# Optimization experiments

Hardware: AMD Instinct MI355X
Metric: run time of the kernel (lower is better)

The kernel has to match this reference:

```python
import jax, jax.numpy as jnp
import numpy as np

DIM = 1024
NUM_HEADS = 16
HEAD_DIM = DIM // NUM_HEADS
SCALE = HEAD_DIM ** (-0.5)


def setup_inputs() -> dict:
    key = jax.random.key(0)
    k_x, k_qkv, k_ow, k_ob = jax.random.split(key, 4)
    x = jax.random.normal(k_x, (4, 2048, DIM), dtype=jnp.float32)
    # nn.Linear(dim, 3*dim, bias=False): store as [dim, 3*dim] for x @ W
    w_qkv = jax.random.normal(k_qkv, (DIM, 3 * DIM), dtype=jnp.float32) * (DIM ** -0.5)
    w_out = jax.random.normal(k_ow, (DIM, DIM), dtype=jnp.float32) * (DIM ** -0.5)
    b_out = jax.random.normal(k_ob, (DIM,), dtype=jnp.float32) * 0.02
    return {"x": x, "w_qkv": w_qkv, "w_out": w_out, "b_out": b_out}


def reference(x, w_qkv, w_out, b_out):
    B, S, D = x.shape
    H, Hd = NUM_HEADS, HEAD_DIM
    qkv = x @ w_qkv                                  # [B, S, 3*D]
    # rearrange 'b s (v h d) -> v b h s d'
    qkv = qkv.reshape(B, S, 3, H, Hd).transpose(2, 0, 3, 1, 4)
    q, k, v = qkv[0], qkv[1], qkv[2]                 # each [B, H, S, Hd]
    scores = jnp.einsum('bhqd,bhkd->bhqk', q, k) * SCALE
    attn = jax.nn.softmax(scores, axis=-1)
    out = jnp.einsum('bhqk,bhkd->bhqd', attn, v)     # [B, H, S, Hd]
    out = out.transpose(0, 2, 1, 3).reshape(B, S, D)  # 'b h s d -> b s (h d)'
    return out @ w_out + b_out
```

## Files before the change

### kernel.cpp

```cpp
#include <hip/hip_runtime.h>
#include <hip/hip_bf16.h>
#include <stdint.h>

typedef __bf16 bf16_t;
typedef __bf16 bf16x4 __attribute__((ext_vector_type(4)));
typedef __bf16 bf16x8 __attribute__((ext_vector_type(8)));
typedef float f32x4 __attribute__((ext_vector_type(4)));
typedef unsigned short u16;

#define L2E 1.4426950408889634f
#define MC 69.249473f

__device__ __forceinline__ void async_load16(const bf16_t* g, bf16_t* l) {
  __builtin_amdgcn_global_load_lds(
      (__attribute__((address_space(1))) uint32_t*)g,
      (__attribute__((address_space(3))) uint32_t*)l, 16, 0, 0);
}

__global__ void detect_k(const uint16_t* __restrict__ x, int* __restrict__ flag) {
  if (threadIdx.x == 0 && blockIdx.x == 0) {
    int bad = 0;
    for (int i = 0; i < 256; ++i) {
      uint16_t h = x[2 * i];
      int e = (h >> 7) & 0xFF;
      if (e == 0 || e >= 0xBD) bad++;
    }
    *flag = (bad > 32) ? 1 : 0;
  }
}

__global__ void convert_k(const void* __restrict__ in, bf16_t* __restrict__ out,
                          int n, const int* __restrict__ flag) {
  const int f = *flag;
  const int i0 = blockIdx.x * blockDim.x + threadIdx.x;
  const int stride = gridDim.x * blockDim.x;
  if (f) {
    const float* p = (const float*)in;
    for (int i = i0; i < n; i += stride) {
      float v = p[i];
      v = (v == v) ? v : 0.f;
      v = fminf(fmaxf(v, -1e6f), 1e6f);
      out[i] = (bf16_t)v;
    }
  } else {
    const bf16_t* p = (const bf16_t*)in;
    for (int i = i0; i < n; i += stride) {
      float v = (float)p[i];
      v = (v == v) ? v : 0.f;
      v = fminf(fmaxf(v, -1e6f), 1e6f);
      out[i] = (bf16_t)v;
    }
  }
}

__global__ __launch_bounds__(256) void wtrans_k(const void* __restrict__ in,
                                                bf16_t* __restrict__ out, int R,
                                                int C, const int* __restrict__ flag) {
  __shared__ u16 tile[64][65];
  const int f = *flag;
  const int tr = blockIdx.y * 64, tc = blockIdx.x * 64;
  const int t = threadIdx.x;
#pragma unroll
  for (int i = 0; i < 16; ++i) {
    int idx = i * 256 + t, r = idx >> 6, c = idx & 63;
    float v;
    if (f)
      v = ((const float*)in)[(size_t)(tr + r) * C + tc + c];
    else
      v = (float)((const bf16_t*)in)[(size_t)(tr + r) * C + tc + c];
    v = (v == v) ? v : 0.f;
    v = fminf(fmaxf(v, -1e6f), 1e6f);
    bf16_t b = (bf16_t)v;
    tile[r][c] = *(u16*)&b;
  }
  __syncthreads();
#pragma unroll
  for (int i = 0; i < 16; ++i) {
    int idx = i * 256 + t, r = idx >> 6, c = idx & 63;
    ((u16*)out)[(size_t)(tc + r) * R + tr + c] = tile[c][r];
  }
}

__device__ __forceinline__ void gemm_bt_mainloop(
    const bf16_t* __restrict__ A, const bf16_t* __restrict__ Bt, int K, int m0,
    int n0, bf16_t* As, bf16_t* Bs, f32x4 acc[4][4]) {
  const int t = threadIdx.x, lane = t & 63, w = t >> 6;
  const int l15 = lane & 15, quad = lane >> 4;
  const int wm = (w >> 1) * 64, wn = (w & 1) * 64;
  const int srow = w * 16 + (lane >> 2);
  const int sk = (lane & 3) * 8;
  const bf16_t* gA = A + (size_t)(m0 + srow) * K + sk;
  const bf16_t* gB = Bt + (size_t)(n0 + srow) * K + sk;
  bf16_t* lA = As + w * 512;
  bf16_t* lB = Bs + w * 512;
  const size_t gstep = (size_t)64 * K;

  for (int kt = 0; kt < K; kt += 32) {
    __syncthreads();
    async_load16(gA, lA);
    async_load16(gA + gstep, lA + 2048);
    async_load16(gB, lB);
    async_load16(gB + gstep, lB + 2048);
    gA += 32;
    gB += 32;
    __syncthreads();
    bf16x8 af[4], bfr[4];
#pragma unroll
    for (int f = 0; f < 4; ++f) {
      af[f] = *(const bf16x8*)(As + (wm + f * 16 + l15) * 32 + quad * 8);
      bfr[f] = *(const bf16x8*)(Bs + (wn + f * 16 + l15) * 32 + quad * 8);
    }
#pragma unroll
    for (int i = 0; i < 4; ++i)
#pragma unroll
      for (int j = 0; j < 4; ++j)
        acc[i][j] =
            __builtin_amdgcn_mfma_f32_16x16x32_bf16(af[i], bfr[j], acc[i][j], 0, 0, 0);
  }
}

__global__ __launch_bounds__(256) void qkv_gemm_k(const bf16_t* __restrict__ X,
                                                  const bf16_t* __restrict__ WqT,
                                                  bf16_t* __restrict__ qo,
                                                  bf16_t* __restrict__ ko,
                                                  bf16_t* __restrict__ vo) {
  __shared__ __align__(16) bf16_t As[128 * 32];
  __shared__ __align__(16) bf16_t Bs[128 * 32];
  const int m0 = blockIdx.y * 128, n0 = blockIdx.x * 128;
  f32x4 acc[4][4];
  const f32x4 z = {0.f, 0.f, 0.f, 0.f};
#pragma unroll
  for (int i = 0; i < 4; ++i)
#pragma unroll
    for (int j = 0; j < 4; ++j) acc[i][j] = z;
  gemm_bt_mainloop(X, WqT, 1024, m0, n0, As, Bs, acc);

  const int lane = threadIdx.x & 63, w = threadIdx.x >> 6;
  const int l15 = lane & 15, quad = lane >> 4;
  const int wm = (w >> 1) * 64, wn = (w & 1) * 64;
#pragma unroll
  for (int j = 0; j < 4; ++j) {
    const int gnb = n0 + wn + j * 16;
    const int vi = gnb >> 10;
    const int rem = gnb & 1023;
    const int h = rem >> 6;
    const int d = (rem & 63) + l15;
    const float scale = (vi == 0) ? 0.125f : 1.0f;
    bf16_t* dst = (vi == 0) ? qo : ((vi == 1) ? ko : vo);
#pragma unroll
    for (int i = 0; i < 4; ++i) {
#pragma unroll
      for (int r = 0; r < 4; ++r) {
        const int gm = m0 + wm + i * 16 + quad * 4 + r;
        const int b = gm >> 11, s = gm & 2047;
        dst[(((size_t)(b * 16 + h) * 2048 + s) << 6) + d] =
            (bf16_t)(acc[i][j][r] * scale);
      }
    }
  }
}

__global__ __launch_bounds__(256) void vtrans_k(const u16* __restrict__ in,
                                                u16* __restrict__ out) {
  __shared__ u16 tile[64][65];
  const int bh = blockIdx.y, st = blockIdx.x;
  const u16* src = in + ((size_t)bh * 2048 + st * 64) * 64;
  u16* dst = out + (size_t)bh * 64 * 2048 + st * 64;
  const int t = threadIdx.x;
#pragma unroll
  for (int i = 0; i < 16; ++i) {
    int idx = i * 256 + t, r = idx >> 6, c = idx & 63;
    tile[r][c] = src[(size_t)r * 64 + c];
  }
  __syncthreads();
#pragma unroll
  for (int i = 0; i < 16; ++i) {
    int idx = i * 256 + t, r = idx >> 6, c = idx & 63;
    dst[(size_t)r * 2048 + c] = tile[c][r];
  }
}

__global__ __launch_bounds__(256) void out_gemm_k(const bf16_t* __restrict__ Ain,
                                                  const bf16_t* __restrict__ WoT,
                                                  const bf16_t* __restrict__ bias,
                                                  void* __restrict__ outp,
                                                  const int* __restrict__ flag) {
  __shared__ __align__(16) bf16_t As[128 * 32];
  __shared__ __align__(16) bf16_t Bs[128 * 32];
  const int m0 = blockIdx.y * 128, n0 = blockIdx.x * 128;
  f32x4 acc[4][4];
  const f32x4 z = {0.f, 0.f, 0.f, 0.f};
#pragma unroll
  for (int i = 0; i < 4; ++i)
#pragma unroll
    for (int j = 0; j < 4; ++j) acc[i][j] = z;
  gemm_bt_mainloop(Ain, WoT, 1024, m0, n0, As, Bs, acc);

  const int f32out = *flag;
  const int lane = threadIdx.x & 63, w = threadIdx.x >> 6;
  const int l15 = lane & 15, quad = lane >> 4;
  const int wm = (w >> 1) * 64, wn = (w & 1) * 64;
#pragma unroll
  for (int j = 0; j < 4; ++j) {
    const int gn = n0 + wn + j * 16 + l15;
    const float bv = (float)bias[gn];
#pragma unroll
    for (int i = 0; i < 4; ++i) {
#pragma unroll
      for (int r = 0; r < 4; ++r) {
        const int gm = m0 + wm + i * 16 + quad * 4 + r;
        const float val = acc[i][j][r] + bv;
        if (f32out)
          ((float*)outp)[(size_t)gm * 1024 + gn] = val;
        else
          ((bf16_t*)outp)[(size_t)gm * 1024 + gn] = (bf16_t)val;
      }
    }
  }
}

#define KTILE 4096

__global__ __launch_bounds__(256) void attn_k(const bf16_t* __restrict__ q,
                                              const bf16_t* __restrict__ k,
                                              const bf16_t* __restrict__ vt,
                                              bf16_t* __restrict__ o) {
  __shared__ __align__(16) bf16_t Ps[64 * 64];
  __shared__ __align__(16) bf16_t Ks[2 * KTILE];
  __shared__ __align__(16) bf16_t Vts[2 * KTILE];

  const int t = threadIdx.x, lane = t & 63, w = t >> 6;
  const int l15 = lane & 15, quad = lane >> 4;
  const int x = blockIdx.x;
  const int j = x >> 3;
  const int bh = (x & 7) * 8 + (j >> 5);
  const int qt = j & 31;
  const bf16_t* qp = q + ((size_t)bh * 2048 + qt * 64) * 64;
  const bf16_t* kp = k + (size_t)bh * 2048 * 64;
  const bf16_t* vp = vt + (size_t)bh * 64 * 2048;

  const int lane8 = lane >> 3, lc = lane & 7;
  int kOff[2], vOff[2], ldsOff[2];
#pragma unroll
  for (int c = 0; c < 2; ++c) {
    const int rho = (w * 2 + c) * 8 + lane8;
    const int srow = (rho >> 4) + (rho & 15) * 4;
    const int col = (lc ^ (rho & 7)) * 8;
    kOff[c] = srow * 64 + col;
    vOff[c] = rho * 2048 + col;
    ldsOff[c] = (w * 2 + c) * 512;
  }

#pragma unroll
  for (int c = 0; c < 2; ++c) {
    async_load16(kp + kOff[c], Ks + ldsOff[c]);
    async_load16(vp + vOff[c], Vts + ldsOff[c]);
  }
#pragma unroll
  for (int p = 0; p < 2; ++p) {
    const int off = p * 2048 + w * 512 + lane * 8;
    async_load16(qp + off, Ps + off);
  }
  __syncthreads();

  bf16x8 qf[2];
#pragma unroll
  for (int ks = 0; ks < 2; ++ks)
    qf[ks] = *(const bf16x8*)(Ps + (w * 16 + l15) * 64 + ks * 32 + quad * 8);

  f32x4 acc[4];
  const f32x4 z = {0.f, 0.f, 0.f, 0.f};
  float lsum[4];
#pragma unroll
  for (int f = 0; f < 4; ++f) {
    acc[f] = z;
    lsum[f] = 0.f;
  }

  bf16_t* psw = Ps + w * 1024;

  for (int kt = 0; kt < 32; ++kt) {
    const int b = kt & 1;
    if (kt < 31) {
      const int bn = b ^ 1;
#pragma unroll
      for (int c = 0; c < 2; ++c) {
        async_load16(kp + (size_t)(kt + 1) * KTILE + kOff[c],
                     Ks + bn * KTILE + ldsOff[c]);
        async_load16(vp + (size_t)(kt + 1) * 64 + vOff[c],
                     Vts + bn * KTILE + ldsOff[c]);
      }
    }

    const bf16_t* Kb = Ks + b * KTILE;
    const bf16_t* Vb = Vts + b * KTILE;

    f32x4 sacc[4];
#pragma unroll
    for (int f = 0; f < 4; ++f) sacc[f] = z;
#pragma unroll
    for (int ks = 0; ks < 2; ++ks) {
      const int cx = (((ks * 4 + quad) ^ (l15 & 7)) * 8);
      bf16x8 kf[4];
#pragma unroll
      for (int f = 0; f < 4; ++f)
        kf[f] = *(const bf16x8*)(Kb + (f * 16 + l15) * 64 + cx);
      __builtin_amdgcn_s_setprio(1);
#pragma unroll
      for (int f = 0; f < 4; ++f)
        sacc[f] = __builtin_amdgcn_mfma_f32_16x16x32_bf16(qf[ks], kf[f],
                                                          sacc[f], 0, 0, 0);
      __builtin_amdgcn_s_setprio(0);
    }

#pragma unroll
    for (int r = 0; r < 4; ++r) {
      bf16x4 pk;
      float ls = 0.f;
#pragma unroll
      for (int f = 0; f < 4; ++f) {
        const float pv =
            __builtin_amdgcn_exp2f(fminf(fmaf(sacc[f][r], L2E, -MC), 0.f));
        ls += pv;
        pk[f] = (bf16_t)pv;
      }
      lsum[r] += ls;
      const int row = quad * 4 + r;
      *(bf16x4*)(psw + row * 64 + ((l15 >> 1) ^ (row & 7)) * 8 +
                 (l15 & 1) * 4) = pk;
    }

#pragma unroll
    for (int ks = 0; ks < 2; ++ks) {
      const int cx = (((ks * 4 + quad) ^ (l15 & 7)) * 8);
      bf16x8 vf[4];
#pragma unroll
      for (int f = 0; f < 4; ++f)
        vf[f] = *(const bf16x8*)(Vb + (f * 16 + l15) * 64 + cx);
      bf16x8 pf = *(const bf16x8*)(psw + l15 * 64 +
                                   ((ks * 4 + quad) ^ (l15 & 7)) * 8);
      __builtin_amdgcn_s_setprio(1);
#pragma unroll
      for (int f = 0; f < 4; ++f)
        acc[f] = __builtin_amdgcn_mfma_f32_16x16x32_bf16(pf, vf[f], acc[f], 0,
                                                         0, 0);
      __builtin_amdgcn_s_setprio(0);
    }

    if (kt < 31) __syncthreads();
  }

#pragma unroll
  for (int r = 0; r < 4; ++r) {
    float s = lsum[r];
    s += __shfl_xor(s, 1, 64);
    s += __shfl_xor(s, 2, 64);
    s += __shfl_xor(s, 4, 64);
    s += __shfl_xor(s, 8, 64);
    lsum[r] = 1.0f / fmaxf(s, 1e-37f);
  }

  const int b = bh >> 4, h = bh & 15;
#pragma unroll
  for (int r = 0; r < 4; ++r) {
    const int srow = qt * 64 + w * 16 + quad * 4 + r;
    const float inv = lsum[r];
#pragma unroll
    for (int f = 0; f < 4; ++f) {
      const int d = f * 16 + l15;
      o[(size_t)(b * 2048 + srow) * 1024 + h * 64 + d] =
          (bf16_t)(acc[f][r] * inv);
    }
  }
}

extern "C" void kernel_launch(void* const* d_in, const int* in_sizes, int n_in,
                              void* d_out, int out_size, void* d_ws, size_t ws_size,
                              hipStream_t stream) {
  const void* x_raw = d_in[0];
  const void* wqkv_raw = d_in[1];
  const void* wout_raw = d_in[2];
  const void* bout_raw = d_in[3];

  const int nx = 4 * 2048 * 1024;
  const int nwq = 1024 * 3072;
  const int nwo = 1024 * 1024;
  const int nb = 1024;

  char* ws = (char*)d_ws;
  int* flag = (int*)ws;
  bf16_t* xb = (bf16_t*)(ws + 256);
  bf16_t* wqbT = xb + nx;
  bf16_t* wobT = wqbT + nwq;
  bf16_t* bob = wobT + nwo;
  bf16_t* qb = bob + nb;
  const size_t bhsd = (size_t)4 * 16 * 2048 * 64;
  bf16_t* kb = qb + bhsd;
  bf16_t* vb = kb + bhsd;
  bf16_t* vtb = xb;
  bf16_t* ab = vb;

  detect_k<<<1, 64, 0, stream>>>((const uint16_t*)x_raw, flag);
  convert_k<<<2048, 256, 0, stream>>>(x_raw, xb, nx, flag);
  wtrans_k<<<dim3(3072 / 64, 1024 / 64), 256, 0, stream>>>(wqkv_raw, wqbT, 1024,
                                                           3072, flag);
  wtrans_k<<<dim3(1024 / 64, 1024 / 64), 256, 0, stream>>>(wout_raw, wobT, 1024,
                                                           1024, flag);
  convert_k<<<4, 256, 0, stream>>>(bout_raw, bob, nb, flag);

  qkv_gemm_k<<<dim3(3072 / 128, 8192 / 128), 256, 0, stream>>>(xb, wqbT, qb, kb, vb);
  vtrans_k<<<dim3(32, 64), 256, 0, stream>>>((const u16*)vb, (u16*)vtb);
  attn_k<<<dim3(2048), 256, 0, stream>>>(qb, kb, vtb, ab);
  out_gemm_k<<<dim3(1024 / 128, 8192 / 128), 256, 0, stream>>>(ab, wobT, bob,
                                                               d_out, flag);
}
```

Measured before the change: 337.0 us.

## Write V transposed directly from QKV GEMM epilogue and drop vtrans kernel

The QKV GEMM epilogue now stores the V slice straight into the [b,h,d,s] transposed layout with 4-element vector stores along the sequence axis. This removes the separate vtrans_k launch and its extra read and write of the whole V tensor. The workspace buffers are remapped so the attention output reuses the x buffer. The attention kernel also gets a launch-bounds occupancy hint of 4 blocks per CU, which may limit registers and cause spills.

```diff
diff --git a/kernel.cpp b/kernel.cpp
--- a/kernel.cpp
+++ b/kernel.cpp
@@ -123,7 +123,7 @@
                                                   const bf16_t* __restrict__ WqT,
                                                   bf16_t* __restrict__ qo,
                                                   bf16_t* __restrict__ ko,
-                                                  bf16_t* __restrict__ vo) {
+                                                  bf16_t* __restrict__ vto) {
   __shared__ __align__(16) bf16_t As[128 * 32];
   __shared__ __align__(16) bf16_t Bs[128 * 32];
   const int m0 = blockIdx.y * 128, n0 = blockIdx.x * 128;
@@ -145,38 +145,30 @@
     const int rem = gnb & 1023;
     const int h = rem >> 6;
     const int d = (rem & 63) + l15;
-    const float scale = (vi == 0) ? 0.125f : 1.0f;
-    bf16_t* dst = (vi == 0) ? qo : ((vi == 1) ? ko : vo);
-#pragma unroll
-    for (int i = 0; i < 4; ++i) {
-#pragma unroll
-      for (int r = 0; r < 4; ++r) {
-        const int gm = m0 + wm + i * 16 + quad * 4 + r;
-        const int b = gm >> 11, s = gm & 2047;
-        dst[(((size_t)(b * 16 + h) * 2048 + s) << 6) + d] =
-            (bf16_t)(acc[i][j][r] * scale);
+    if (vi == 2) {
+#pragma unroll
+      for (int i = 0; i < 4; ++i) {
+        const int gm0 = m0 + wm + i * 16 + quad * 4;
+        const int b = gm0 >> 11, s = gm0 & 2047;
+        bf16x4 pv;
+#pragma unroll
+        for (int r = 0; r < 4; ++r) pv[r] = (bf16_t)acc[i][j][r];
+        *(bf16x4*)(vto + ((size_t)(b * 16 + h) * 64 + d) * 2048 + s) = pv;
       }
-    }
-  }
-}
-
-__global__ __launch_bounds__(256) void vtrans_k(const u16* __restrict__ in,
-                                                u16* __restrict__ out) {
-  __shared__ u16 tile[64][65];
-  const int bh = blockIdx.y, st = blockIdx.x;
-  const u16* src = in + ((size_t)bh * 2048 + st * 64) * 64;
-  u16* dst = out + (size_t)bh * 64 * 2048 + st * 64;
-  const int t = threadIdx.x;
-#pragma unroll
-  for (int i = 0; i < 16; ++i) {
-    int idx = i * 256 + t, r = idx >> 6, c = idx & 63;
-    tile[r][c] = src[(size_t)r * 64 + c];
-  }
-  __syncthreads();
-#pragma unroll
-  for (int i = 0; i < 16; ++i) {
-    int idx = i * 256 + t, r = idx >> 6, c = idx & 63;
-    dst[(size_t)r * 2048 + c] = tile[c][r];
+    } else {
+      const float scale = (vi == 0) ? 0.125f : 1.0f;
+      bf16_t* dst = (vi == 0) ? qo : ko;
+#pragma unroll
+      for (int i = 0; i < 4; ++i) {
+#pragma unroll
+        for (int r = 0; r < 4; ++r) {
+          const int gm = m0 + wm + i * 16 + quad * 4 + r;
+          const int b = gm >> 11, s = gm & 2047;
+          dst[(((size_t)(b * 16 + h) * 2048 + s) << 6) + d] =
+              (bf16_t)(acc[i][j][r] * scale);
+        }
+      }
+    }
   }
 }
 
@@ -221,10 +213,10 @@
 
 #define KTILE 4096
 
-__global__ __launch_bounds__(256) void attn_k(const bf16_t* __restrict__ q,
-                                              const bf16_t* __restrict__ k,
-                                              const bf16_t* __restrict__ vt,
-                                              bf16_t* __restrict__ o) {
+__global__ __launch_bounds__(256, 4) void attn_k(const bf16_t* __restrict__ q,
+                                                 const bf16_t* __restrict__ k,
+                                                 const bf16_t* __restrict__ vt,
+                                                 bf16_t* __restrict__ o) {
   __shared__ __align__(16) bf16_t Ps[64 * 64];
   __shared__ __align__(16) bf16_t Ks[2 * KTILE];
   __shared__ __align__(16) bf16_t Vts[2 * KTILE];
@@ -396,9 +388,8 @@
   bf16_t* qb = bob + nb;
   const size_t bhsd = (size_t)4 * 16 * 2048 * 64;
   bf16_t* kb = qb + bhsd;
-  bf16_t* vb = kb + bhsd;
-  bf16_t* vtb = xb;
-  bf16_t* ab = vb;
+  bf16_t* vtb = kb + bhsd;
+  bf16_t* ab = xb;
 
   detect_k<<<1, 64, 0, stream>>>((const uint16_t*)x_raw, flag);
   convert_k<<<2048, 256, 0, stream>>>(x_raw, xb, nx, flag);
@@ -408,8 +399,8 @@
                                                            1024, flag);
   convert_k<<<4, 256, 0, stream>>>(bout_raw, bob, nb, flag);
 
-  qkv_gemm_k<<<dim3(3072 / 128, 8192 / 128), 256, 0, stream>>>(xb, wqbT, qb, kb, vb);
-  vtrans_k<<<dim3(32, 64), 256, 0, stream>>>((const u16*)vb, (u16*)vtb);
+  qkv_gemm_k<<<dim3(3072 / 128, 8192 / 128), 256, 0, stream>>>(xb, wqbT, qb, kb,
+                                                               vtb);
   attn_k<<<dim3(2048), 256, 0, stream>>>(qb, kb, vtb, ab);
   out_gemm_k<<<dim3(1024 / 128, 8192 / 128), 256, 0, stream>>>(ab, wobT, bob,
                                                                d_out, flag);
```

Measured after the change: 317.1 us. -5.9%, faster.
